# Kernel optimization log

Hardware: AMD Instinct MI355X
Metric: run time of the kernel (lower is better)

Reference implementation:

```python
import jax, jax.numpy as jnp
import numpy as np

H = 50  # hidden_size

def setup_inputs() -> dict:
    key = jax.random.key(0)
    ks = jax.random.split(key, 7)
    B, T = 2048, 1024
    s = 1.0 / np.sqrt(H)  # PyTorch default init scale
    return {
        "x": jax.random.normal(ks[0], (B, T, 1), dtype=jnp.float32),
        "W_ih": jax.random.uniform(ks[1], (4 * H, 1), jnp.float32, -s, s),
        "W_hh": jax.random.uniform(ks[2], (4 * H, H), jnp.float32, -s, s),
        "b_ih": jax.random.uniform(ks[3], (4 * H,), jnp.float32, -s, s),
        "b_hh": jax.random.uniform(ks[4], (4 * H,), jnp.float32, -s, s),
        "W_lin": jax.random.uniform(ks[5], (1, H), jnp.float32, -s, s),
        "b_lin": jax.random.uniform(ks[6], (1,), jnp.float32, -s, s),
    }

def reference(x, W_ih, W_hh, b_ih, b_hh, W_lin, b_lin):
    B, T, _ = x.shape
    # Precompute input contribution to gates for all timesteps: [T, B, 4H]
    gx = jnp.einsum('bti,gi->tbg', x, W_ih) + (b_ih + b_hh)

    def step(carry, gx_t):
        h, c = carry
        gates = gx_t + h @ W_hh.T               # [B, 4H]
        i, f, g, o = jnp.split(gates, 4, axis=-1)  # PyTorch gate order i,f,g,o
        i = jax.nn.sigmoid(i)
        f = jax.nn.sigmoid(f)
        g = jnp.tanh(g)
        o = jax.nn.sigmoid(o)
        c = f * c + i * g
        h = o * jnp.tanh(c)
        return (h, c), None

    h0 = jnp.zeros((B, H), x.dtype)
    c0 = jnp.zeros((B, H), x.dtype)
    (h_last, _), _ = jax.lax.scan(step, (h0, c0), gx)
    # Linear head on last timestep's hidden state -> [B, 1]
    return h_last @ W_lin.T + b_lin
```

## Files before the change

kernel.cpp:

```cpp
#include <hip/hip_runtime.h>


#define H     50
#define TT    1024
#define BATCH 2048
#define BW    4
#define NTHR  256
#define NTILE 4
#define KP    80

typedef float    f32x4 __attribute__((ext_vector_type(4)));
typedef _Float16 f16x8 __attribute__((ext_vector_type(8)));

__global__ __launch_bounds__(NTHR, 2) void lstm_kernel(
    const float* __restrict__ x,
    const float* __restrict__ W_ih,
    const float* __restrict__ W_hh,
    const float* __restrict__ b_ih,
    const float* __restrict__ b_hh,
    const float* __restrict__ W_lin,
    const float* __restrict__ b_lin,
    float* __restrict__ out)
{
    __shared__ _Float16 hb[2][BW][KP];
    __shared__ float    XT[TT + 2][BW];
    __shared__ float    redH[H][BW];

    const int tid  = threadIdx.x;
    const int wave = tid >> 6;
    const int lane = tid & 63;
    const int L15  = lane & 15;
    const int kq   = lane >> 4;
    const int bl   = L15 & 3;
    const int b0   = blockIdx.x * BW;

    const float LOG2E  = 1.4426950408889634f;
    const float LOG2E2 = 2.8853900817779268f;

    f16x8 A[NTILE][2];
    #pragma unroll
    for (int tt = 0; tt < NTILE; ++tt) {
        const int m  = (NTILE * wave + tt) * 16 + L15;
        const int jm = m >> 2, gm = m & 3;
        const bool v = (jm < H);
        const float s = (gm == 2) ? LOG2E2 : -LOG2E;
        #pragma unroll
        for (int kf = 0; kf < 2; ++kf) {
            f16x8 vv;
            #pragma unroll
            for (int e = 0; e < 8; ++e) {
                const int k = kf * 32 + kq * 8 + e;
                _Float16 val = (_Float16)0.f;
                if (v && k < H) val = (_Float16)(s * W_hh[(gm * H + jm) * H + k]);
                vv[e] = val;
            }
            A[tt][kf] = vv;
        }
    }

    const int  j  = 16 * wave + 4 * (L15 >> 2) + kq;
    const bool jv = (j < H);
    const float wlin = jv ? W_lin[j] : 0.f;
    float zw[4], zb[4];
    #pragma unroll
    for (int r = 0; r < 4; ++r) {
        const float s = (r == 2) ? LOG2E2 : -LOG2E;
        zw[r] = jv ? s * W_ih[r * H + j] : 0.f;
        zb[r] = jv ? s * (b_ih[r * H + j] + b_hh[r * H + j]) : 0.f;
    }

    for (int i = tid; i < 2 * BW * KP; i += NTHR)
        ((_Float16*)hb)[i] = (_Float16)0.f;
    for (int i = tid; i < TT * BW; i += NTHR) {
        const int bb = i >> 10, t = i & 1023;
        XT[t][bb] = x[(size_t)(b0 + bb) * TT + t];
    }
    if (tid < 2 * BW) ((float*)&XT[TT][0])[tid] = 0.f;

    float c2 = 0.f;
    float hlast = 0.f;
    __syncthreads();

    float xt_cur = XT[0][bl];
    const bool s0 = (L15 & 4) != 0;
    const bool s1 = (L15 & 8) != 0;

    #pragma unroll 1
    for (int tbase = 0; tbase < TT; tbase += 2) {
        #pragma unroll
        for (int half = 0; half < 2; ++half) {
            const int t = tbase + half;
            const _Float16* hp = &hb[half][bl][0];
            _Float16*       np = &hb[half ^ 1][bl][0];

            const f16x8 B0 = *(const f16x8*)(hp + kq * 8);
            const f16x8 B1 = *(const f16x8*)(hp + 32 + kq * 8);

            f32x4 zc;
            #pragma unroll
            for (int r = 0; r < 4; ++r)
                zc[r] = __builtin_fmaf(zw[r], xt_cur, zb[r]);

            f32x4 a0 = __builtin_amdgcn_mfma_f32_16x16x32_f16(A[0][0], B0, zc, 0, 0, 0);
            f32x4 a1 = __builtin_amdgcn_mfma_f32_16x16x32_f16(A[1][0], B0, zc, 0, 0, 0);
            f32x4 a2 = __builtin_amdgcn_mfma_f32_16x16x32_f16(A[2][0], B0, zc, 0, 0, 0);
            f32x4 a3 = __builtin_amdgcn_mfma_f32_16x16x32_f16(A[3][0], B0, zc, 0, 0, 0);
            a0 = __builtin_amdgcn_mfma_f32_16x16x32_f16(A[0][1], B1, a0, 0, 0, 0);
            a1 = __builtin_amdgcn_mfma_f32_16x16x32_f16(A[1][1], B1, a1, 0, 0, 0);
            a2 = __builtin_amdgcn_mfma_f32_16x16x32_f16(A[2][1], B1, a2, 0, 0, 0);
            a3 = __builtin_amdgcn_mfma_f32_16x16x32_f16(A[3][1], B1, a3, 0, 0, 0);

            xt_cur = XT[t + 1][bl];

            float g[4];
            #pragma unroll
            for (int r = 0; r < 4; ++r) {
                const float m01 = s0 ? a1[r] : a0[r];
                const float m23 = s0 ? a3[r] : a2[r];
                g[r] = s1 ? m23 : m01;
            }

            const float Ei = __builtin_amdgcn_exp2f(g[0]);
            const float Ef = __builtin_amdgcn_exp2f(g[1]);
            const float Eg = __builtin_amdgcn_exp2f(g[2]);
            const float Eo = __builtin_amdgcn_exp2f(g[3]);
            const float P  = (1.0f + Ei) * (1.0f + Eg);
            const float Q  = 1.0f + Ef;
            const float Q2 = __builtin_fmaf(LOG2E2, Ef, LOG2E2);
            const float num = __builtin_fmaf(c2, P, (Eg - 1.0f) * Q2);
            c2 = num * __builtin_amdgcn_rcpf(P * Q);
            const float ca = fminf(c2, 80.0f);
            const float Ec = __builtin_amdgcn_exp2f(ca);
            const float h  = (Ec - 1.0f) *
                __builtin_amdgcn_rcpf((1.0f + Eo) * (1.0f + Ec));
            hlast = h;

            np[j] = (_Float16)h;
            __syncthreads();
        }
    }

    if (jv) redH[j][bl] = wlin * hlast;
    __syncthreads();
    if (tid < BW) {
        float s = b_lin[0];
        #pragma unroll 10
        for (int jj = 0; jj < H; ++jj) s += redH[jj][tid];
        out[b0 + tid] = s;
    }
}

extern "C" void kernel_launch(void* const* d_in, const int* in_sizes, int n_in,
                              void* d_out, int out_size, void* d_ws, size_t ws_size,
                              hipStream_t stream) {
    const float* x     = (const float*)d_in[0];
    const float* W_ih  = (const float*)d_in[1];
    const float* W_hh  = (const float*)d_in[2];
    const float* b_ih  = (const float*)d_in[3];
    const float* b_hh  = (const float*)d_in[4];
    const float* W_lin = (const float*)d_in[5];
    const float* b_lin = (const float*)d_in[6];
    float* out = (float*)d_out;

    dim3 grid(BATCH / BW);
    dim3 block(NTHR);
    lstm_kernel<<<grid, block, 0, stream>>>(x, W_ih, W_hh, b_ih, b_hh,
                                            W_lin, b_lin, out);
}
```

Before: 338.7 us.

## Process eight batch rows per block using full MFMA columns with permuted hidden layout

Result: slower. 428.0 us (+26.4%).

```diff
diff --git a/kernel.cpp b/kernel.cpp
--- a/kernel.cpp
+++ b/kernel.cpp
@@ -4,7 +4,7 @@
 #define H     50
 #define TT    1024
 #define BATCH 2048
-#define BW    4
+#define BW    8
 #define NTHR  256
 #define NTILE 4
 #define KP    80
@@ -12,7 +12,7 @@
 typedef float    f32x4 __attribute__((ext_vector_type(4)));
 typedef _Float16 f16x8 __attribute__((ext_vector_type(8)));
 
-__global__ __launch_bounds__(NTHR, 2) void lstm_kernel(
+__global__ __launch_bounds__(NTHR, 1) void lstm_kernel(
     const float* __restrict__ x,
     const float* __restrict__ W_ih,
     const float* __restrict__ W_hh,
@@ -23,15 +23,15 @@
     float* __restrict__ out)
 {
     __shared__ _Float16 hb[2][BW][KP];
-    __shared__ float    XT[TT + 2][BW];
-    __shared__ float    redH[H][BW];
+    __shared__ float    redW[4][BW];
 
     const int tid  = threadIdx.x;
     const int wave = tid >> 6;
     const int lane = tid & 63;
     const int L15  = lane & 15;
     const int kq   = lane >> 4;
-    const int bl   = L15 & 3;
+    const int rp   = L15 >> 3;
+    const int bl   = L15 & 7;
     const int b0   = blockIdx.x * BW;
 
     const float LOG2E  = 1.4426950408889634f;
@@ -40,8 +40,9 @@
     f16x8 A[NTILE][2];
     #pragma unroll
     for (int tt = 0; tt < NTILE; ++tt) {
-        const int m  = (NTILE * wave + tt) * 16 + L15;
-        const int jm = m >> 2, gm = m & 3;
+        const int tg = NTILE * wave + tt;
+        const int jm = 4 * tg + (L15 >> 2);
+        const int gm = L15 & 3;
         const bool v = (jm < H);
         const float s = (gm == 2) ? LOG2E2 : -LOG2E;
         #pragma unroll
@@ -49,41 +50,44 @@
             f16x8 vv;
             #pragma unroll
             for (int e = 0; e < 8; ++e) {
-                const int k = kf * 32 + kq * 8 + e;
+                const int kap = kf * 32 + kq * 8 + e;
+                const int u = 16 * (kap >> 4) + 4 * ((kap >> 1) & 1)
+                            + ((kap >> 2) & 3) + 8 * (kap & 1);
                 _Float16 val = (_Float16)0.f;
-                if (v && k < H) val = (_Float16)(s * W_hh[(gm * H + jm) * H + k]);
+                if (v && u < H) val = (_Float16)(s * W_hh[(gm * H + jm) * H + u]);
                 vv[e] = val;
             }
             A[tt][kf] = vv;
         }
     }
 
-    const int  j  = 16 * wave + 4 * (L15 >> 2) + kq;
-    const bool jv = (j < H);
-    const float wlin = jv ? W_lin[j] : 0.f;
-    float zw[4], zb[4];
+    const int  uA  = 16 * wave + 4 * rp + kq;
+    const int  uB  = uA + 8;
+    const bool vA  = (uA < H);
+    const bool vB  = (uB < H);
+    float zwA[4], zbA[4], zwB[4], zbB[4];
     #pragma unroll
     for (int r = 0; r < 4; ++r) {
         const float s = (r == 2) ? LOG2E2 : -LOG2E;
-        zw[r] = jv ? s * W_ih[r * H + j] : 0.f;
-        zb[r] = jv ? s * (b_ih[r * H + j] + b_hh[r * H + j]) : 0.f;
+        zwA[r] = vA ? s * W_ih[r * H + uA] : 0.f;
+        zbA[r] = vA ? s * (b_ih[r * H + uA] + b_hh[r * H + uA]) : 0.f;
+        zwB[r] = vB ? s * W_ih[r * H + uB] : 0.f;
+        zbB[r] = vB ? s * (b_ih[r * H + uB] + b_hh[r * H + uB]) : 0.f;
     }
+    const float wlA = vA ? W_lin[uA] : 0.f;
+    const float wlB = vB ? W_lin[uB] : 0.f;
+
+    const int sw = 16 * wave + 2 * (2 * kq + rp);
+
+    const float* xg = x + (size_t)(b0 + bl) * TT;
 
     for (int i = tid; i < 2 * BW * KP; i += NTHR)
         ((_Float16*)hb)[i] = (_Float16)0.f;
-    for (int i = tid; i < TT * BW; i += NTHR) {
-        const int bb = i >> 10, t = i & 1023;
-        XT[t][bb] = x[(size_t)(b0 + bb) * TT + t];
-    }
-    if (tid < 2 * BW) ((float*)&XT[TT][0])[tid] = 0.f;
 
-    float c2 = 0.f;
-    float hlast = 0.f;
+    float c2A = 0.f, c2B = 0.f;
+    float hA = 0.f, hB = 0.f;
+    float xcur = xg[0];
     __syncthreads();
-
-    float xt_cur = XT[0][bl];
-    const bool s0 = (L15 & 4) != 0;
-    const bool s1 = (L15 & 8) != 0;
 
     #pragma unroll 1
     for (int tbase = 0; tbase < TT; tbase += 2) {
@@ -96,57 +100,74 @@
             const f16x8 B0 = *(const f16x8*)(hp + kq * 8);
             const f16x8 B1 = *(const f16x8*)(hp + 32 + kq * 8);
 
-            f32x4 zc;
-            #pragma unroll
-            for (int r = 0; r < 4; ++r)
-                zc[r] = __builtin_fmaf(zw[r], xt_cur, zb[r]);
-
-            f32x4 a0 = __builtin_amdgcn_mfma_f32_16x16x32_f16(A[0][0], B0, zc, 0, 0, 0);
-            f32x4 a1 = __builtin_amdgcn_mfma_f32_16x16x32_f16(A[1][0], B0, zc, 0, 0, 0);
-            f32x4 a2 = __builtin_amdgcn_mfma_f32_16x16x32_f16(A[2][0], B0, zc, 0, 0, 0);
-            f32x4 a3 = __builtin_amdgcn_mfma_f32_16x16x32_f16(A[3][0], B0, zc, 0, 0, 0);
+            const f32x4 zz = {0.f, 0.f, 0.f, 0.f};
+            f32x4 a0 = __builtin_amdgcn_mfma_f32_16x16x32_f16(A[0][0], B0, zz, 0, 0, 0);
+            f32x4 a1 = __builtin_amdgcn_mfma_f32_16x16x32_f16(A[1][0], B0, zz, 0, 0, 0);
+            f32x4 a2 = __builtin_amdgcn_mfma_f32_16x16x32_f16(A[2][0], B0, zz, 0, 0, 0);
+            f32x4 a3 = __builtin_amdgcn_mfma_f32_16x16x32_f16(A[3][0], B0, zz, 0, 0, 0);
             a0 = __builtin_amdgcn_mfma_f32_16x16x32_f16(A[0][1], B1, a0, 0, 0, 0);
             a1 = __builtin_amdgcn_mfma_f32_16x16x32_f16(A[1][1], B1, a1, 0, 0, 0);
             a2 = __builtin_amdgcn_mfma_f32_16x16x32_f16(A[2][1], B1, a2, 0, 0, 0);
             a3 = __builtin_amdgcn_mfma_f32_16x16x32_f16(A[3][1], B1, a3, 0, 0, 0);
 
-            xt_cur = XT[t + 1][bl];
+            const float xnxt = xg[(t + 1) & (TT - 1)];
 
-            float g[4];
+            const bool rb = (rp != 0);
+            float ga[4], gb[4];
             #pragma unroll
             for (int r = 0; r < 4; ++r) {
-                const float m01 = s0 ? a1[r] : a0[r];
-                const float m23 = s0 ? a3[r] : a2[r];
-                g[r] = s1 ? m23 : m01;
+                ga[r] = (rb ? a1[r] : a0[r]) + __builtin_fmaf(zwA[r], xcur, zbA[r]);
+                gb[r] = (rb ? a3[r] : a2[r]) + __builtin_fmaf(zwB[r], xcur, zbB[r]);
             }
 
-            const float Ei = __builtin_amdgcn_exp2f(g[0]);
-            const float Ef = __builtin_amdgcn_exp2f(g[1]);
-            const float Eg = __builtin_amdgcn_exp2f(g[2]);
-            const float Eo = __builtin_amdgcn_exp2f(g[3]);
-            const float P  = (1.0f + Ei) * (1.0f + Eg);
-            const float Q  = 1.0f + Ef;
-            const float Q2 = __builtin_fmaf(LOG2E2, Ef, LOG2E2);
-            const float num = __builtin_fmaf(c2, P, (Eg - 1.0f) * Q2);
-            c2 = num * __builtin_amdgcn_rcpf(P * Q);
-            const float ca = fminf(c2, 80.0f);
-            const float Ec = __builtin_amdgcn_exp2f(ca);
-            const float h  = (Ec - 1.0f) *
-                __builtin_amdgcn_rcpf((1.0f + Eo) * (1.0f + Ec));
-            hlast = h;
+            {
+                const float Ei = __builtin_amdgcn_exp2f(ga[0]);
+                const float Ef = __builtin_amdgcn_exp2f(ga[1]);
+                const float Eg = __builtin_amdgcn_exp2f(ga[2]);
+                const float Eo = __builtin_amdgcn_exp2f(ga[3]);
+                const float P  = (1.0f + Ei) * (1.0f + Eg);
+                const float Q  = 1.0f + Ef;
+                const float Q2 = __builtin_fmaf(LOG2E2, Ef, LOG2E2);
+                const float num = __builtin_fmaf(c2A, P, (Eg - 1.0f) * Q2);
+                c2A = num * __builtin_amdgcn_rcpf(P * Q);
+                const float ca = fminf(c2A, 80.0f);
+                const float Ec = __builtin_amdgcn_exp2f(ca);
+                hA = (Ec - 1.0f) * __builtin_amdgcn_rcpf((1.0f + Eo) * (1.0f + Ec));
+            }
+            {
+                const float Ei = __builtin_amdgcn_exp2f(gb[0]);
+                const float Ef = __builtin_amdgcn_exp2f(gb[1]);
+                const float Eg = __builtin_amdgcn_exp2f(gb[2]);
+                const float Eo = __builtin_amdgcn_exp2f(gb[3]);
+                const float P  = (1.0f + Ei) * (1.0f + Eg);
+                const float Q  = 1.0f + Ef;
+                const float Q2 = __builtin_fmaf(LOG2E2, Ef, LOG2E2);
+                const float num = __builtin_fmaf(c2B, P, (Eg - 1.0f) * Q2);
+                c2B = num * __builtin_amdgcn_rcpf(P * Q);
+                const float ca = fminf(c2B, 80.0f);
+                const float Ec = __builtin_amdgcn_exp2f(ca);
+                hB = (Ec - 1.0f) * __builtin_amdgcn_rcpf((1.0f + Eo) * (1.0f + Ec));
+            }
 
-            np[j] = (_Float16)h;
+            const _Float16 fA = (_Float16)hA;
+            const _Float16 fB = (_Float16)hB;
+            const unsigned int pk =
+                (unsigned int)__builtin_bit_cast(unsigned short, fA) |
+                ((unsigned int)__builtin_bit_cast(unsigned short, fB) << 16);
+            *(unsigned int*)(np + sw) = pk;
             __syncthreads();
+            xcur = xnxt;
         }
     }
 
-    if (jv) redH[j][bl] = wlin * hlast;
+    float p = __builtin_fmaf(wlA, hA, wlB * hB);
+    #pragma unroll
+    for (int m = 8; m <= 32; m <<= 1) p += __shfl_xor(p, m, 64);
+    if (lane < BW) redW[wave][lane] = p;
     __syncthreads();
     if (tid < BW) {
-        float s = b_lin[0];
-        #pragma unroll 10
-        for (int jj = 0; jj < H; ++jj) s += redH[jj][tid];
-        out[b0 + tid] = s;
+        out[b0 + tid] = b_lin[0] + redW[0][tid] + redW[1][tid]
+                      + redW[2][tid] + redW[3][tid];
     }
 }
 
```
